# Kernel optimization log

Measured on AMD Instinct MI355X. Metric: run time of the kernel, lower is better.

## Reference

```python
import jax, jax.numpy as jnp
import numpy as np

N = 100000      # nodes
E = 1600000     # random edges (self loops added in reference, like add_self_loops)
D_IN = 128
D_OUT = 128
NEG_SLOPE = 0.01  # F.leaky_relu default in the torch source


def setup_inputs() -> dict:
    key = jax.random.key(0)
    k_x, k_e, k_w, k_b, k_a, k_ab = jax.random.split(key, 6)
    x = jax.random.normal(k_x, (N, D_IN), dtype=jnp.float32)
    edge_index = jax.random.randint(k_e, (2, E), 0, N, dtype=jnp.int32)
    # small init scales keep exp(score) in a sane range (torch default init is also small)
    W_lin = jax.random.normal(k_w, (D_OUT, D_IN), dtype=jnp.float32) * 0.05
    b_lin = jax.random.normal(k_b, (D_OUT,), dtype=jnp.float32) * 0.05
    W_att = jax.random.normal(k_a, (1, 2 * D_OUT), dtype=jnp.float32) * 0.05
    b_att = jax.random.normal(k_ab, (1,), dtype=jnp.float32) * 0.05
    return {"x": x, "edge_index": edge_index, "W_lin": W_lin, "b_lin": b_lin,
            "W_att": W_att, "b_att": b_att}


def reference(x, edge_index, W_lin, b_lin, W_att, b_att):
    n = x.shape[0]
    d_out = W_lin.shape[0]
    # h = lin(x), computed ONCE (the torch loop redundantly recomputes it per edge)
    h = x @ W_lin.T + b_lin                      # [N, D_OUT]
    # add self loops (pyg_utils.add_self_loops)
    loops = jnp.arange(n, dtype=edge_index.dtype)
    src = jnp.concatenate([edge_index[0], loops])  # node i (attends over its out-neighbors)
    dst = jnp.concatenate([edge_index[1], loops])  # neighbor j
    # attention([h_i ; h_j]) = h_i . a_i + h_j . a_j + b
    a_i = W_att[0, :d_out]
    a_j = W_att[0, d_out:]
    score = h[src] @ a_i + h[dst] @ a_j + b_att[0]           # [E+N]
    score = jnp.where(score >= 0, score, NEG_SLOPE * score)  # leaky_relu(0.01)
    e = jnp.exp(score)                                        # plain exp, as in source (no max-shift)
    denom = jax.ops.segment_sum(e, src, num_segments=n)       # per-source softmax denominator
    alpha = e / denom[src]                                    # [E+N]
    msg = alpha[:, None] * h[dst]                             # [E+N, D_OUT]
    agg = jax.ops.segment_sum(msg, src, num_segments=n)       # attention_matrix @ h
    return jax.nn.elu(agg)
```

## Files before the change

kernel.cpp:

```cpp
#include <hip/hip_runtime.h>
#include <hip/hip_bf16.h>
#include <stdint.h>

typedef unsigned int uint;
typedef unsigned short ushort;

#define D 128
#define NEG_SLOPE 0.01f
#define BN 64
#define CAP 1280
#define NCHUNK 256
#define KMAX 2048

using frag_t = __attribute__((ext_vector_type(8))) short;
using f32x4  = __attribute__((ext_vector_type(4))) float;

__device__ __forceinline__ ushort f2bf(float f) {
    __hip_bfloat16 b = __float2bfloat16(f);
    ushort u; __builtin_memcpy(&u, &b, 2); return u;
}
__device__ __forceinline__ float bflo(uint p) { return __uint_as_float(p << 16); }
__device__ __forceinline__ float bfhi(uint p) { return __uint_as_float(p & 0xffff0000u); }

#define LDK 136

__global__ __launch_bounds__(256) void gemm_h(
    const float* __restrict__ x, const float* __restrict__ W,
    const float* __restrict__ bias, const float* __restrict__ Wa,
    const float* __restrict__ ba,
    ushort* __restrict__ h, float* __restrict__ si, float* __restrict__ sj, int n)
{
    __shared__ ushort xs[64 * LDK];
    __shared__ ushort wsh[128 * LDK];
    const int tid  = threadIdx.x;
    const int row0 = blockIdx.x * 64;

    {
        const int r = tid >> 5;
        const int k = (tid & 31) * 4;
#pragma unroll
        for (int i = 0; i < 8; ++i) {
            int lr = r + 8 * i;
            int gr = row0 + lr;
            int cr = gr < n ? gr : (n - 1);
            float4 v = *(const float4*)(x + (size_t)cr * D + k);
            ushort4 u; u.x = f2bf(v.x); u.y = f2bf(v.y); u.z = f2bf(v.z); u.w = f2bf(v.w);
            *(ushort4*)&xs[lr * LDK + k] = u;
        }
#pragma unroll
        for (int i = 0; i < 16; ++i) {
            int lr = r + 8 * i;
            float4 v = *(const float4*)(W + (size_t)lr * D + k);
            ushort4 u; u.x = f2bf(v.x); u.y = f2bf(v.y); u.z = f2bf(v.z); u.w = f2bf(v.w);
            *(ushort4*)&wsh[lr * LDK + k] = u;
        }
    }
    __syncthreads();

    const int wv   = tid >> 6;
    const int lane = tid & 63;
    const int mr   = lane & 15;
    const int qk   = (lane >> 4) * 8;

    f32x4 acc[8] = {};
    const ushort* xrow = xs + (16 * wv + mr) * LDK;
#pragma unroll
    for (int kk = 0; kk < 4; ++kk) {
        frag_t a = *(const frag_t*)(xrow + kk * 32 + qk);
#pragma unroll
        for (int t = 0; t < 8; ++t) {
            frag_t bf = *(const frag_t*)(wsh + (16 * t + mr) * LDK + kk * 32 + qk);
            acc[t] = __builtin_amdgcn_mfma_f32_16x16x32_bf16(a, bf, acc[t], 0, 0, 0);
        }
    }

    const int crow = 16 * wv + (lane >> 4) * 4;
    float pi[4] = {0.f, 0.f, 0.f, 0.f};
    float pj[4] = {0.f, 0.f, 0.f, 0.f};
#pragma unroll
    for (int t = 0; t < 8; ++t) {
        int col = 16 * t + mr;
        float bb = bias[col];
        float av = Wa[col];
        float bv = Wa[D + col];
#pragma unroll
        for (int r = 0; r < 4; ++r) {
            float v = acc[t][r] + bb;
            int grow = row0 + crow + r;
            if (grow < n) h[(size_t)grow * D + col] = f2bf(v);
            pi[r] += v * av;
            pj[r] += v * bv;
        }
    }
#pragma unroll
    for (int o = 1; o < 16; o <<= 1) {
#pragma unroll
        for (int r = 0; r < 4; ++r) {
            pi[r] += __shfl_xor(pi[r], o);
            pj[r] += __shfl_xor(pj[r], o);
        }
    }
    if (mr == 0) {
        float bav = ba[0];
#pragma unroll
        for (int r = 0; r < 4; ++r) {
            int grow = row0 + crow + r;
            if (grow < n) { si[grow] = pi[r] + bav; sj[grow] = pj[r]; }
        }
    }
}

__global__ __launch_bounds__(256) void count_k(
    const int* __restrict__ src, int* __restrict__ counts, int e, int K, int cpb)
{
    __shared__ int hist[KMAX];
    const int c = blockIdx.x;
    for (int i = threadIdx.x; i < K; i += 256) hist[i] = 0;
    __syncthreads();
    const int beg = c * cpb;
    const int end = min(e, beg + cpb);
    for (int i = beg + threadIdx.x; i < end; i += 256)
        atomicAdd(&hist[src[i] >> 6], 1);
    __syncthreads();
    for (int i = threadIdx.x; i < K; i += 256) counts[c * K + i] = hist[i];
}

__global__ __launch_bounds__(NCHUNK) void scan_chunks(
    int* __restrict__ counts, int* __restrict__ total, int K)
{
    __shared__ int s[NCHUNK];
    const int b = blockIdx.x, t = threadIdx.x;
    int v = counts[t * K + b];
    s[t] = v; __syncthreads();
#pragma unroll
    for (int o = 1; o < NCHUNK; o <<= 1) {
        int tv = (t >= o) ? s[t - o] : 0;
        __syncthreads();
        s[t] += tv;
        __syncthreads();
    }
    counts[t * K + b] = s[t] - v;
    if (t == NCHUNK - 1) total[b] = s[t];
}

__global__ __launch_bounds__(256) void fill_k(
    const int* __restrict__ src, const int* __restrict__ dst,
    const int* __restrict__ cbase, uint* __restrict__ barr,
    int e, int K, int cpb)
{
    __shared__ int cur[KMAX];
    const int c = blockIdx.x;
    for (int i = threadIdx.x; i < K; i += 256) cur[i] = cbase[c * K + i];
    __syncthreads();
    const int beg = c * cpb;
    const int end = min(e, beg + cpb);
    for (int i = beg + threadIdx.x; i < end; i += 256) {
        int s = src[i], d = dst[i];
        int b = s >> 6;
        int p = atomicAdd(&cur[b], 1);
        if (p < CAP)
            barr[(size_t)b * CAP + p] = ((uint)(s & (BN - 1)) << 17) | (uint)d;
    }
}

__global__ __launch_bounds__(512) void agg_k(
    const ushort* __restrict__ h, const uint* __restrict__ barr,
    const int* __restrict__ total,
    const float* __restrict__ si, const float* __restrict__ sj,
    float* __restrict__ out, int n)
{
    __shared__ uint2 se[CAP];
    __shared__ int hist[BN];
    __shared__ int base[BN];
    __shared__ int cur[BN];
    __shared__ float si_s[BN];
    __shared__ float sj_s[BN];
    const int b    = blockIdx.x;
    const int tid  = threadIdx.x;
    const int lane = tid & 63;
    const int wv   = tid >> 6;
    const int node0 = b << 6;

    if (tid < BN) {
        hist[tid] = 0;
        int nd = node0 + tid;
        si_s[tid] = nd < n ? si[nd] : 0.f;
        sj_s[tid] = nd < n ? sj[nd] : 0.f;
    }
    __syncthreads();

    const int ecnt = min(total[b], CAP);
    const uint* eb = barr + (size_t)b * CAP;

    uint p0 = 0, p1 = 0, p2 = 0;
    float w0 = 0.f, w1 = 0.f, w2 = 0.f;
    const bool v0 = tid < ecnt, v1 = tid + 512 < ecnt, v2 = tid + 1024 < ecnt;
    if (v0) {
        p0 = eb[tid];
        float sc = si_s[p0 >> 17] + sj[p0 & 0x1FFFFu];
        sc = sc >= 0.f ? sc : NEG_SLOPE * sc;
        w0 = __expf(sc);
        atomicAdd(&hist[p0 >> 17], 1);
    }
    if (v1) {
        p1 = eb[tid + 512];
        float sc = si_s[p1 >> 17] + sj[p1 & 0x1FFFFu];
        sc = sc >= 0.f ? sc : NEG_SLOPE * sc;
        w1 = __expf(sc);
        atomicAdd(&hist[p1 >> 17], 1);
    }
    if (v2) {
        p2 = eb[tid + 1024];
        float sc = si_s[p2 >> 17] + sj[p2 & 0x1FFFFu];
        sc = sc >= 0.f ? sc : NEG_SLOPE * sc;
        w2 = __expf(sc);
        atomicAdd(&hist[p2 >> 17], 1);
    }
    __syncthreads();

    if (tid < 64) {
        int v = hist[tid];
        int s = v;
#pragma unroll
        for (int o = 1; o < 64; o <<= 1) {
            int t = __shfl_up(s, o);
            if (lane >= o) s += t;
        }
        base[tid] = s - v;
        cur[tid]  = s - v;
    }
    __syncthreads();

    if (v0) se[atomicAdd(&cur[p0 >> 17], 1)] = make_uint2(p0, __float_as_uint(w0));
    if (v1) se[atomicAdd(&cur[p1 >> 17], 1)] = make_uint2(p1, __float_as_uint(w1));
    if (v2) se[atomicAdd(&cur[p2 >> 17], 1)] = make_uint2(p2, __float_as_uint(w2));
    __syncthreads();

    const uint lo = (uint)lane << 1;
#pragma unroll 1
    for (int t = 0; t < 8; ++t) {
        const int ls = (wv << 3) + t;
        const int node = node0 + ls;
        if (node >= n) break;

        float sc = si_s[ls] + sj_s[ls];
        sc = sc >= 0.f ? sc : NEG_SLOPE * sc;
        float w_ = __expf(sc);
        uint hv = *(const uint*)(h + (((uint)node << 7) + lo));
        float a0 = w_ * bflo(hv), a1 = w_ * bfhi(hv);
        float denom = w_;

        const int c = hist[ls];
        const uint2* seg = se + base[ls];
        int j = 0;
        for (; j + 8 <= c; j += 8) {
            uint2 ww[8];
#pragma unroll
            for (int i = 0; i < 8; ++i) ww[i] = seg[j + i];
            uint gg[8];
#pragma unroll
            for (int i = 0; i < 8; ++i)
                gg[i] = *(const uint*)(h + (((ww[i].x & 0x1FFFFu) << 7) + lo));
#pragma unroll
            for (int i = 0; i < 8; ++i) {
                float ei = __uint_as_float(ww[i].y);
                denom += ei;
                a0 += ei * bflo(gg[i]);
                a1 += ei * bfhi(gg[i]);
            }
        }
        if (j + 4 <= c) {
            uint2 ww[4];
#pragma unroll
            for (int i = 0; i < 4; ++i) ww[i] = seg[j + i];
            uint gg[4];
#pragma unroll
            for (int i = 0; i < 4; ++i)
                gg[i] = *(const uint*)(h + (((ww[i].x & 0x1FFFFu) << 7) + lo));
#pragma unroll
            for (int i = 0; i < 4; ++i) {
                float ei = __uint_as_float(ww[i].y);
                denom += ei;
                a0 += ei * bflo(gg[i]);
                a1 += ei * bfhi(gg[i]);
            }
            j += 4;
        }
        for (; j < c; ++j) {
            uint2 w = seg[j];
            uint g = *(const uint*)(h + (((w.x & 0x1FFFFu) << 7) + lo));
            float we = __uint_as_float(w.y);
            denom += we;
            a0 += we * bflo(g);
            a1 += we * bfhi(g);
        }

        float inv = 1.f / denom;
        a0 *= inv; a1 *= inv;
        a0 = a0 > 0.f ? a0 : expm1f(a0);
        a1 = a1 > 0.f ? a1 : expm1f(a1);
        *(float2*)(out + (((uint)node << 7) + lo)) = make_float2(a0, a1);
    }
}

extern "C" void kernel_launch(void* const* d_in, const int* in_sizes, int n_in,
                              void* d_out, int out_size, void* d_ws, size_t ws_size,
                              hipStream_t stream)
{
    const float* x  = (const float*)d_in[0];
    const int*   ei = (const int*)  d_in[1];
    const float* Wl = (const float*)d_in[2];
    const float* bl = (const float*)d_in[3];
    const float* Wa = (const float*)d_in[4];
    const float* ba = (const float*)d_in[5];
    const int n = in_sizes[0] / D;
    const int e = in_sizes[1] / 2;
    const int* src = ei;
    const int* dst = ei + e;

    const int K   = (n + BN - 1) / BN;
    const int cpb = (e + NCHUNK - 1) / NCHUNK;

    char* w = (char*)d_ws;
    size_t off = 0;
    ushort* h      = (ushort*)(w + off); off += (size_t)n * D * 2;
    float*  si     = (float*) (w + off); off += (size_t)n * 4;
    float*  sj     = (float*) (w + off); off += (size_t)n * 4;
    int*    counts = (int*)   (w + off); off += (size_t)NCHUNK * K * 4;
    int*    total  = (int*)   (w + off); off += ((size_t)K * 4 + 15) & ~(size_t)15;
    uint*   barr   = (uint*)  (w + off); off += (size_t)K * CAP * 4;

    gemm_h      <<<(n + 63) / 64, 256,    0, stream>>>(x, Wl, bl, Wa, ba, h, si, sj, n);
    count_k     <<<NCHUNK,        256,    0, stream>>>(src, counts, e, K, cpb);
    scan_chunks <<<K,             NCHUNK, 0, stream>>>(counts, total, K);
    fill_k      <<<NCHUNK,        256,    0, stream>>>(src, dst, counts, barr, e, K, cpb);
    agg_k       <<<K,             512,    0, stream>>>(h, barr, total, si, sj, (float*)d_out, n);
}
```

Before: 249.3 us.

## Fuse edge-count histogram into GEMM kernel and raise chunk count

The separate count kernel is merged into the GEMM kernel. Its first NCHUNK blocks build per-chunk source-bucket histograms in reused shared memory after the matmul, which removes one launch. The GEMM tile grows to 128 rows with 512 threads, and the chunk count rises to 768 so the count and fill phases spread over more blocks. The aggregation inner loop is reduced from an 8-way plus 4-way unroll to a 4-way unroll with tree-summed partials. The scan kernel now runs with 768 threads per block and a longer serial scan, and the counts array grows to match.

Result: no change. 244.9 us (-1.7%).

```diff
diff --git a/kernel.cpp b/kernel.cpp
--- a/kernel.cpp
+++ b/kernel.cpp
@@ -9,7 +9,7 @@
 #define NEG_SLOPE 0.01f
 #define BN 64
 #define CAP 1280
-#define NCHUNK 256
+#define NCHUNK 768
 #define KMAX 2048
 
 using frag_t = __attribute__((ext_vector_type(8))) short;
@@ -24,23 +24,25 @@
 
 #define LDK 136
 
-__global__ __launch_bounds__(256) void gemm_h(
+__global__ __launch_bounds__(512) void gemm_h(
     const float* __restrict__ x, const float* __restrict__ W,
     const float* __restrict__ bias, const float* __restrict__ Wa,
     const float* __restrict__ ba,
-    ushort* __restrict__ h, float* __restrict__ si, float* __restrict__ sj, int n)
-{
-    __shared__ ushort xs[64 * LDK];
+    ushort* __restrict__ h, float* __restrict__ si, float* __restrict__ sj,
+    const int* __restrict__ src, int* __restrict__ counts,
+    int n, int e, int K, int cpb)
+{
+    __shared__ ushort xs[128 * LDK];
     __shared__ ushort wsh[128 * LDK];
     const int tid  = threadIdx.x;
-    const int row0 = blockIdx.x * 64;
+    const int row0 = blockIdx.x * 128;
 
     {
         const int r = tid >> 5;
         const int k = (tid & 31) * 4;
 #pragma unroll
         for (int i = 0; i < 8; ++i) {
-            int lr = r + 8 * i;
+            int lr = r + 16 * i;
             int gr = row0 + lr;
             int cr = gr < n ? gr : (n - 1);
             float4 v = *(const float4*)(x + (size_t)cr * D + k);
@@ -48,8 +50,8 @@
             *(ushort4*)&xs[lr * LDK + k] = u;
         }
 #pragma unroll
-        for (int i = 0; i < 16; ++i) {
-            int lr = r + 8 * i;
+        for (int i = 0; i < 8; ++i) {
+            int lr = r + 16 * i;
             float4 v = *(const float4*)(W + (size_t)lr * D + k);
             ushort4 u; u.x = f2bf(v.x); u.y = f2bf(v.y); u.z = f2bf(v.z); u.w = f2bf(v.w);
             *(ushort4*)&wsh[lr * LDK + k] = u;
@@ -73,6 +75,7 @@
             acc[t] = __builtin_amdgcn_mfma_f32_16x16x32_bf16(a, bf, acc[t], 0, 0, 0);
         }
     }
+    __syncthreads();
 
     const int crow = 16 * wv + (lane >> 4) * 4;
     float pi[4] = {0.f, 0.f, 0.f, 0.f};
@@ -108,21 +111,19 @@
             if (grow < n) { si[grow] = pi[r] + bav; sj[grow] = pj[r]; }
         }
     }
-}
-
-__global__ __launch_bounds__(256) void count_k(
-    const int* __restrict__ src, int* __restrict__ counts, int e, int K, int cpb)
-{
-    __shared__ int hist[KMAX];
+
     const int c = blockIdx.x;
-    for (int i = threadIdx.x; i < K; i += 256) hist[i] = 0;
-    __syncthreads();
-    const int beg = c * cpb;
-    const int end = min(e, beg + cpb);
-    for (int i = beg + threadIdx.x; i < end; i += 256)
-        atomicAdd(&hist[src[i] >> 6], 1);
-    __syncthreads();
-    for (int i = threadIdx.x; i < K; i += 256) counts[c * K + i] = hist[i];
+    if (c < NCHUNK) {
+        int* hist = (int*)xs;
+        for (int i = tid; i < K; i += 512) hist[i] = 0;
+        __syncthreads();
+        const int beg = c * cpb;
+        const int end = min(e, beg + cpb);
+        for (int i = beg + tid; i < end; i += 512)
+            atomicAdd(&hist[src[i] >> 6], 1);
+        __syncthreads();
+        for (int i = tid; i < K; i += 512) counts[c * K + i] = hist[i];
+    }
 }
 
 __global__ __launch_bounds__(NCHUNK) void scan_chunks(
@@ -143,18 +144,18 @@
     if (t == NCHUNK - 1) total[b] = s[t];
 }
 
-__global__ __launch_bounds__(256) void fill_k(
+__global__ __launch_bounds__(512) void fill_k(
     const int* __restrict__ src, const int* __restrict__ dst,
     const int* __restrict__ cbase, uint* __restrict__ barr,
     int e, int K, int cpb)
 {
     __shared__ int cur[KMAX];
     const int c = blockIdx.x;
-    for (int i = threadIdx.x; i < K; i += 256) cur[i] = cbase[c * K + i];
+    for (int i = threadIdx.x; i < K; i += 512) cur[i] = cbase[c * K + i];
     __syncthreads();
     const int beg = c * cpb;
     const int end = min(e, beg + cpb);
-    for (int i = beg + threadIdx.x; i < end; i += 256) {
+    for (int i = beg + threadIdx.x; i < end; i += 512) {
         int s = src[i], d = dst[i];
         int b = s >> 6;
         int p = atomicAdd(&cur[b], 1);
@@ -253,38 +254,17 @@
         const int c = hist[ls];
         const uint2* seg = se + base[ls];
         int j = 0;
-        for (; j + 8 <= c; j += 8) {
-            uint2 ww[8];
-#pragma unroll
-            for (int i = 0; i < 8; ++i) ww[i] = seg[j + i];
-            uint gg[8];
-#pragma unroll
-            for (int i = 0; i < 8; ++i)
-                gg[i] = *(const uint*)(h + (((ww[i].x & 0x1FFFFu) << 7) + lo));
-#pragma unroll
-            for (int i = 0; i < 8; ++i) {
-                float ei = __uint_as_float(ww[i].y);
-                denom += ei;
-                a0 += ei * bflo(gg[i]);
-                a1 += ei * bfhi(gg[i]);
-            }
-        }
-        if (j + 4 <= c) {
-            uint2 ww[4];
-#pragma unroll
-            for (int i = 0; i < 4; ++i) ww[i] = seg[j + i];
-            uint gg[4];
-#pragma unroll
-            for (int i = 0; i < 4; ++i)
-                gg[i] = *(const uint*)(h + (((ww[i].x & 0x1FFFFu) << 7) + lo));
-#pragma unroll
-            for (int i = 0; i < 4; ++i) {
-                float ei = __uint_as_float(ww[i].y);
-                denom += ei;
-                a0 += ei * bflo(gg[i]);
-                a1 += ei * bfhi(gg[i]);
-            }
-            j += 4;
+        for (; j + 4 <= c; j += 4) {
+            uint2 w0_ = seg[j], w1_ = seg[j + 1], w2_ = seg[j + 2], w3_ = seg[j + 3];
+            uint g0 = *(const uint*)(h + (((w0_.x & 0x1FFFFu) << 7) + lo));
+            uint g1 = *(const uint*)(h + (((w1_.x & 0x1FFFFu) << 7) + lo));
+            uint g2 = *(const uint*)(h + (((w2_.x & 0x1FFFFu) << 7) + lo));
+            uint g3 = *(const uint*)(h + (((w3_.x & 0x1FFFFu) << 7) + lo));
+            float e0 = __uint_as_float(w0_.y), e1 = __uint_as_float(w1_.y);
+            float e2 = __uint_as_float(w2_.y), e3 = __uint_as_float(w3_.y);
+            denom += (e0 + e1) + (e2 + e3);
+            a0 += e0 * bflo(g0) + e1 * bflo(g1) + e2 * bflo(g2) + e3 * bflo(g3);
+            a1 += e0 * bfhi(g0) + e1 * bfhi(g1) + e2 * bfhi(g2) + e3 * bfhi(g3);
         }
         for (; j < c; ++j) {
             uint2 w = seg[j];
@@ -330,9 +310,11 @@
     int*    total  = (int*)   (w + off); off += ((size_t)K * 4 + 15) & ~(size_t)15;
     uint*   barr   = (uint*)  (w + off); off += (size_t)K * CAP * 4;
 
-    gemm_h      <<<(n + 63) / 64, 256,    0, stream>>>(x, Wl, bl, Wa, ba, h, si, sj, n);
-    count_k     <<<NCHUNK,        256,    0, stream>>>(src, counts, e, K, cpb);
-    scan_chunks <<<K,             NCHUNK, 0, stream>>>(counts, total, K);
-    fill_k      <<<NCHUNK,        256,    0, stream>>>(src, dst, counts, barr, e, K, cpb);
-    agg_k       <<<K,             512,    0, stream>>>(h, barr, total, si, sj, (float*)d_out, n);
-}
+    const int gblocks = (n + 127) / 128;
+
+    gemm_h      <<<gblocks, 512,    0, stream>>>(x, Wl, bl, Wa, ba, h, si, sj,
+                                                 src, counts, n, e, K, cpb);
+    scan_chunks <<<K,       NCHUNK, 0, stream>>>(counts, total, K);
+    fill_k      <<<NCHUNK,  512,    0, stream>>>(src, dst, counts, barr, e, K, cpb);
+    agg_k       <<<K,       512,    0, stream>>>(h, barr, total, si, sj, (float*)d_out, n);
+}
```
